# Optimization experiments

Measured on AMD Instinct MI355X. Metric: run time of the kernel, lower is better.

The kernel has to match this reference:

```python
import jax, jax.numpy as jnp
import numpy as np

# ---- static dims (from init_kwargs) ----
B, V, G, NH, C = 2, 3, 2, 8, 128
CPG, CH, HPG = C // G, C // NH, NH // G          # 64, 16, 4
Hq = Wq = 32
D = 4                                            # bev_depth_dim
Hk, Wk = Hq // 2, Wq * D                         # 16, 128 (per rearrange)
NS = Hk * Wk                                     # n_sample = 2048
Hi = Wi = 64
SCALE = CH ** -0.5
OFR = 5.0                                        # offset_range_factor
EPS = 1e-5


def grid_sample_bilinear(img, grid):
    """torch.F.grid_sample(mode='bilinear', align_corners=True, padding='zeros').
    img: (N, Cc, H, W); grid: (N, Hg, Wg, 2) with (x, y) in [-1, 1]."""
    N, Cc, H, W = img.shape
    x = (grid[..., 0] + 1.0) * 0.5 * (W - 1)
    y = (grid[..., 1] + 1.0) * 0.5 * (H - 1)
    x0 = jnp.floor(x); y0 = jnp.floor(y)
    wx1 = x - x0; wy1 = y - y0
    wx0 = 1.0 - wx1; wy0 = 1.0 - wy1

    def gather(ix, iy):
        valid = ((ix >= 0) & (ix <= W - 1) & (iy >= 0) & (iy <= H - 1)).astype(img.dtype)
        ixc = jnp.clip(ix, 0, W - 1).astype(jnp.int32)
        iyc = jnp.clip(iy, 0, H - 1).astype(jnp.int32)
        vals = jax.vmap(lambda im, yy, xx: im[:, yy, xx])(img, iyc, ixc)  # (N,Cc,Hg,Wg)
        return vals * valid[:, None]

    return (gather(x0, y0) * (wx0 * wy0)[:, None]
            + gather(x0 + 1.0, y0) * (wx1 * wy0)[:, None]
            + gather(x0, y0 + 1.0) * (wx0 * wy1)[:, None]
            + gather(x0 + 1.0, y0 + 1.0) * (wx1 * wy1)[:, None])


def offset_net(qg, w1, b1, gln, bln, w2):
    """Depthwise 1x1 conv (groups=CPG, fan-out D) -> channel LayerNorm -> GELU -> 1x1 conv.
    qg: (B*G, CPG, Hq, Wq) -> (B*G, D, Hq, Wq)."""
    h = qg[:, :, None] * w1.reshape(CPG, D)[None, :, :, None, None] \
        + b1.reshape(CPG, D)[None, :, :, None, None]
    h = h.reshape(B * G, CPG * D, Hq, Wq)
    mu = h.mean(axis=1, keepdims=True)
    var = h.var(axis=1, keepdims=True)           # biased, like torch LayerNorm
    h = (h - mu) * jax.lax.rsqrt(var + EPS) * gln[None, :, None, None] + bln[None, :, None, None]
    h = jax.nn.gelu(h, approximate=False)
    return jnp.einsum('oc,bchw->bohw', w2, h)


def _q_grid():
    gy, gx = jnp.meshgrid(jnp.linspace(-1.0, 1.0, Hq), jnp.linspace(-1.0, 1.0, Wq), indexing='ij')
    return jnp.stack([gy, gx], -1)               # (Hq, Wq, 2) in (y, x)


def setup_inputs() -> dict:
    key = jax.random.key(0)
    ks = jax.random.split(key, 15)
    s = 0.05
    return {
        'x': jax.random.normal(ks[0], (B, V, C, Hi, Wi), jnp.float32),
        'query': jax.random.normal(ks[1], (B, C, Hq, Wq), jnp.float32),
        'reference_points': jax.random.uniform(ks[2], (B, V, Hk, Wk, 2), jnp.float32) * 2.0 - 1.0,
        'off_w1': jax.random.normal(ks[3], (V, CPG * D), jnp.float32) * s,
        'off_b1': jax.random.normal(ks[4], (V, CPG * D), jnp.float32) * s,
        'off_ln_g': jnp.ones((V, CPG * D), jnp.float32),
        'off_ln_b': jnp.zeros((V, CPG * D), jnp.float32),
        'off_w2': jax.random.normal(ks[5], (V, D, CPG * D), jnp.float32) * s,
        'k_w': jax.random.normal(ks[6], (C, C), jnp.float32) * s,
        'k_b': jnp.zeros((C,), jnp.float32),
        'v_w': jax.random.normal(ks[7], (C, C), jnp.float32) * s,
        'v_b': jnp.zeros((C,), jnp.float32),
        'out_w': jax.random.normal(ks[8], (C, C * V), jnp.float32) * s,
        'out_b': jnp.zeros((C,), jnp.float32),
        'rpe_table': jax.random.normal(ks[9], (NH, Hq * 2 - 1, Wq * D * 2 - 1), jnp.float32) * 0.01,
    }


def reference(x, query, reference_points, off_w1, off_b1, off_ln_g, off_ln_b, off_w2,
              k_w, k_b, v_w, v_b, out_w, out_b, rpe_table):
    ref = reference_points[..., ::-1]                     # (x,y) -> (y,x)
    ref = jnp.repeat(ref, G, axis=0)                      # (B*G, V, Hk, Wk, 2)
    q_g = query.reshape(B, G, CPG, Hq, Wq).reshape(B * G, CPG, Hq, Wq)
    q = query.reshape(B * NH, CH, Hq * Wq)
    qg = _q_grid().reshape(1, Hq * Wq, 2)
    off_rng = jnp.array([1.0 / (Hk - 1.0), 1.0 / (Wk - 1.0)], jnp.float32).reshape(1, 2, 1, 1)
    rpe = jnp.broadcast_to(rpe_table[None], (B,) + rpe_table.shape)
    rpe = rpe.reshape(B * G, HPG, rpe_table.shape[1], rpe_table.shape[2])

    outs = []
    for vi in range(V):
        off = offset_net(q_g, off_w1[vi], off_b1[vi], off_ln_g[vi], off_ln_b[vi], off_w2[vi])
        # rearrange '(b g) d (h n) w -> (b g) n h (w d)'
        off = off.reshape(B * G, D, Hk, 2, Wq).transpose(0, 3, 2, 4, 1).reshape(B * G, 2, Hk, Wk)
        off = jnp.tanh(off) * off_rng * OFR
        off = off.transpose(0, 2, 3, 1)                   # (B*G, Hk, Wk, 2) in (y, x)
        rwo = off + ref[:, vi]                            # scale_offset_range=True -> no clamp
        xs = grid_sample_bilinear(x[:, vi].reshape(B * G, CPG, Hi, Wi), rwo[..., ::-1])
        xs = xs.reshape(B, C, NS)
        k = (jnp.einsum('oc,bcn->bon', k_w, xs) + k_b[None, :, None]).reshape(B * NH, CH, NS)
        vv = (jnp.einsum('oc,bcn->bon', v_w, xs) + v_b[None, :, None]).reshape(B * NH, CH, NS)
        attn = jnp.einsum('bcm,bcn->bmn', q, k) * SCALE   # (B*NH, m, NS)
        disp = (qg[:, :, None] - rwo.reshape(B * G, NS, 2)[:, None]) * 0.5  # (B*G, m, NS, 2)
        bias = grid_sample_bilinear(rpe, disp[..., ::-1]).reshape(B * NH, Hq * Wq, NS)
        attn = jax.nn.softmax(attn + bias, axis=-1)
        outs.append(jnp.einsum('bmn,bcn->bcm', attn, vv).reshape(B, C, Hq, Wq))

    out = jnp.concatenate(outs, axis=1)                   # (B, V*C, Hq, Wq)
    return jnp.einsum('oc,bchw->bohw', out_w, out) + out_b[None, :, None, None]
```

## Files before the change

kernel.cpp:

```cpp
#include <hip/hip_runtime.h>
#include <hip/hip_bf16.h>
#include <math.h>


typedef __attribute__((ext_vector_type(8))) short short8;
typedef __attribute__((ext_vector_type(4))) float f32x4;

__device__ __forceinline__ unsigned short f2b(float f){
  unsigned u = __float_as_uint(f);
  return (unsigned short)((u + 0x7FFFu + ((u>>16)&1u)) >> 16);
}
__device__ __forceinline__ unsigned pack2(float lo, float hi){
  return (unsigned)f2b(lo) | ((unsigned)f2b(hi) << 16);
}
__device__ __forceinline__ unsigned cvt_pk_bf16(float lo, float hi){
  unsigned r;
  asm("v_cvt_pk_bf16_f32 %0, %1, %2" : "=v"(r) : "v"(lo), "v"(hi));
  return r;
}

__global__ void k_probe(float* __restrict__ out, float code){
  if(blockIdx.x==0 && threadIdx.x==0) out[0] = code;
}

__global__ __launch_bounds__(256) void k_prep_off(
    const float* __restrict__ query, const float* __restrict__ refp,
    const float* __restrict__ w1, const float* __restrict__ b1,
    const float* __restrict__ lng, const float* __restrict__ lnb,
    const float* __restrict__ w2, float* __restrict__ rwo, float* __restrict__ rws,
    const float* __restrict__ x, float* __restrict__ xt,
    const float* __restrict__ k_w, const float* __restrict__ v_w, const float* __restrict__ out_w,
    unsigned short* __restrict__ kw16, unsigned short* __restrict__ vw16, float* __restrict__ ow_t){
  __shared__ float t[64][65];
  int bx = blockIdx.x;
  if(bx < 3072){
    int wid  = bx*4 + (threadIdx.x>>6);
    int lane = threadIdx.x & 63;
    int vi  = wid >> 12;
    int rem = wid & 4095;
    int bg  = rem >> 10;
    int pix = rem & 1023;
    int y = pix >> 5, xq = pix & 31;
    int b = bg >> 1, g = bg & 1;
    float qv = query[(size_t)(b*128 + g*64 + lane)*1024 + pix];
    float h[4]; float s1 = 0.f, s2 = 0.f;
    #pragma unroll
    for(int d=0; d<4; ++d){
      h[d] = qv*w1[vi*256 + lane*4 + d] + b1[vi*256 + lane*4 + d];
      s1 += h[d]; s2 += h[d]*h[d];
    }
    #pragma unroll
    for(int off=1; off<64; off<<=1){ s1 += __shfl_xor(s1, off); s2 += __shfl_xor(s2, off); }
    float mu   = s1 * (1.f/256.f);
    float var  = s2 * (1.f/256.f) - mu*mu;
    float rstd = rsqrtf(fmaxf(var, 0.f) + 1e-5f);
    float po[4] = {0.f,0.f,0.f,0.f};
    #pragma unroll
    for(int d=0; d<4; ++d){
      float hv = (h[d]-mu)*rstd*lng[vi*256+lane*4+d] + lnb[vi*256+lane*4+d];
      hv = 0.5f*hv*(1.f + erff(hv*0.70710678118654752f));
      #pragma unroll
      for(int o=0; o<4; ++o) po[o] += w2[(vi*4+o)*256 + lane*4 + d] * hv;
    }
    #pragma unroll
    for(int off=1; off<64; off<<=1){
      #pragma unroll
      for(int o=0; o<4; ++o) po[o] += __shfl_xor(po[o], off);
    }
    if(lane == 0){
      int tt = y & 1, hk = y >> 1;
      float rng = tt ? (5.f/127.f) : (5.f/15.f);
      float csc = tt ? 63.5f : 15.5f;
      #pragma unroll
      for(int d=0; d<4; ++d){
        int wk = xq*4 + d;
        float rv = refp[(size_t)(((b*3+vi)*16 + hk)*128 + wk)*2 + (1-tt)];
        float coord = tanhf(po[d])*rng + rv;
        size_t o2 = ((size_t)(vi*4+bg)*2048 + hk*128 + wk)*2 + tt;
        rwo[o2] = coord;
        rws[o2] = coord * csc;
      }
    }
  } else if(bx < 3840){
    int pb = bx - 3072;
    int iy = pb & 63;
    int o2 = pb >> 6;
    const float* src = x + ((size_t)o2*64)*4096 + (size_t)iy*64;
    int ix = threadIdx.x & 63, cq = threadIdx.x >> 6;
    #pragma unroll
    for(int c0 = 0; c0 < 64; c0 += 4)
      t[c0+cq][ix] = src[(size_t)(c0+cq)*4096 + ix];
    __syncthreads();
    float* dst = xt + (((size_t)o2*64 + iy)*64)*64;
    int c = threadIdx.x & 63, xq = threadIdx.x >> 6;
    #pragma unroll
    for(int x0 = 0; x0 < 64; x0 += 4)
      dst[(size_t)(x0+xq)*64 + c] = t[c][x0+xq];
  } else {
    int wb = bx - 3840;
    if(wb < 128){
      int i = (wb & 63)*256 + threadIdx.x;
      if(wb < 64) kw16[i] = f2b(k_w[i]);
      else        vw16[i] = f2b(v_w[i]);
    } else {
      int i = (wb-128)*256 + threadIdx.x;
      if(i < 49152){
        int r = i / 384, c = i - r*384;
        ow_t[c*128 + r] = out_w[i];
      }
    }
  }
}

__global__ __launch_bounds__(256) void k_sampro(
    const float* __restrict__ rwo, const float* __restrict__ xt,
    const unsigned short* __restrict__ kw16, const float* __restrict__ k_b,
    const unsigned short* __restrict__ vw16, const float* __restrict__ v_b,
    unsigned short* __restrict__ k_b16, unsigned short* __restrict__ v_t16){
  __shared__ alignas(16) unsigned short tile[16*136];
  int bx = blockIdx.x;
  int nt = bx & 127;
  int r2 = bx >> 7;
  int b = r2 & 1, vi = r2 >> 1;
  int n0 = nt*16;
  int tid = threadIdx.x, wid = tid>>6, lane = tid&63;
  #pragma unroll
  for(int s = 0; s < 8; ++s){
    int u = wid*8 + s;
    int nl = u >> 1, g = u & 1;
    int n = n0 + nl;
    float yn = rwo[((size_t)(vi*4 + b*2 + g)*2048 + n)*2 + 0];
    float xn = rwo[((size_t)(vi*4 + b*2 + g)*2048 + n)*2 + 1];
    float px = (xn + 1.f)*31.5f;
    float py = (yn + 1.f)*31.5f;
    float x0 = floorf(px), y0 = floorf(py);
    float fx = px - x0, fy = py - y0;
    int ix0 = (int)x0, iy0 = (int)y0;
    const float* base = xt + (size_t)((b*3+vi)*2+g)*4096*64;
    float wts[4] = {(1.f-fx)*(1.f-fy), fx*(1.f-fy), (1.f-fx)*fy, fx*fy};
    int ixs[4] = {ix0, ix0+1, ix0, ix0+1};
    int iys[4] = {iy0, iy0, iy0+1, iy0+1};
    float acc = 0.f;
    #pragma unroll
    for(int tp=0; tp<4; ++tp){
      int ix = ixs[tp], iy = iys[tp];
      if(ix>=0 && ix<64 && iy>=0 && iy<64)
        acc += wts[tp] * base[(size_t)((iy<<6)+ix)*64 + lane];
    }
    tile[nl*136 + g*64 + lane] = f2b(acc);
  }
  __syncthreads();
  int c = lane & 15, qd = lane >> 4;
  short8 af[4];
  #pragma unroll
  for(int kc=0; kc<4; ++kc)
    af[kc] = *(const short8*)(&tile[c*136 + kc*32 + qd*8]);
  size_t vbbase = (size_t)(vi*16 + b*8)*2048*16;
  const float SC2 = 0.36067376022224085f;
  int pbase = ((nt>>1)<<5) + (nt&1);
  #pragma unroll
  for(int half=0; half<2; ++half){
    int nh = wid*2 + half;
    size_t hbase = vbbase + (size_t)nh*2048*16;
    {
      f32x4 C = {0.f,0.f,0.f,0.f};
      #pragma unroll
      for(int kc=0; kc<4; ++kc){
        short8 bf = *(const short8*)(kw16 + (size_t)(nh*16 + c)*128 + kc*32 + qd*8);
        C = __builtin_amdgcn_mfma_f32_16x16x32_bf16(af[kc], bf, C, 0, 0, 0);
      }
      float bias = k_b[nh*16 + c];
      #pragma unroll
      for(int r=0; r<4; ++r)
        k_b16[hbase + (size_t)(n0 + qd*4 + r)*16 + c] = f2b((C[r] + bias)*SC2);
    }
    {
      f32x4 C = {0.f,0.f,0.f,0.f};
      #pragma unroll
      for(int kc=0; kc<4; ++kc){
        short8 bf = *(const short8*)(vw16 + (size_t)(nh*16 + c)*128 + kc*32 + qd*8);
        C = __builtin_amdgcn_mfma_f32_16x16x32_bf16(af[kc], bf, C, 0, 0, 0);
      }
      float bias = v_b[nh*16 + c];
      #pragma unroll
      for(int r=0; r<4; ++r)
        v_t16[hbase + (size_t)c*2048 + pbase + ((qd*4 + r)<<1)] = f2b(C[r] + bias);
    }
  }
}

__global__ __launch_bounds__(256,3) void k_attn(
    const float* __restrict__ rws, const unsigned short* __restrict__ k_b16,
    const unsigned short* __restrict__ v_t16, const float* __restrict__ query,
    const float* __restrict__ rpe, float* __restrict__ attn_pc){
  __shared__ unsigned P32[47*258];
  __shared__ alignas(16) short p_sm[4][16*40];
  int bx = blockIdx.x;
  int vi = bx >> 8;
  int bh = (bx >> 4) & 15;
  int mblk = bx & 15;
  int b = bh >> 3, nh = bh & 7, g = nh >> 2, bg = b*2 + g;
  int tid = threadIdx.x, wid = tid >> 6;
  int lane = tid & 63, c = lane & 15, qd = lane >> 4;
  int m0 = mblk*64 + wid*16;
  float gy0 = -1.f + (2.f/31.f)*(float)(mblk*2);
  float pyL = 15.5f*(gy0 - 4.f/3.f) + 31.f - 0.01f;
  float pyH = 15.5f*(gy0 + 2.f/31.f + 4.f/3.f) + 31.f + 0.01f;
  int a  = max(-1, (int)floorf(pyL));
  int bb = min(63, (int)floorf(pyH));
  int iy_lo = max(a - 1, bb - 46);
  {
    const float* rt = rpe + (size_t)nh*16065;
    for(int e = tid; e < 12126; e += 256){
      int rr = e / 258;
      int cc = e - rr*258;
      int iy = iy_lo + rr;
      int ix = cc - 1;
      bool xv = (ix >= 0) && (ix <= 254);
      float lo = (xv && iy   >= 0 && iy   <= 62) ? rt[iy*255 + ix]     : 0.f;
      float hi = (xv && iy+1 >= 0 && iy+1 <= 62) ? rt[(iy+1)*255 + ix] : 0.f;
      P32[e] = cvt_pk_bf16(lo*1.44269504f, hi*1.44269504f);
    }
  }
  short8 qa;
  #pragma unroll
  for(int j=0; j<8; ++j){
    int ch = qd*8 + j;
    qa[j] = (qd < 2) ? (short)f2b(query[(size_t)(b*128 + nh*16 + ch)*1024 + m0 + c]) : (short)0;
  }
  float Ax2[4];
  #pragma unroll
  for(int r=0; r<4; ++r){
    int mr = m0 + qd*4 + r;
    float gxr = -1.f + (2.f/31.f)*(mr & 31);
    Ax2[r] = 63.5f*gxr + 128.f;
  }
  float gyw = -1.f + (2.f/31.f)*(float)(m0 >> 5);
  float Ay  = 15.5f*gyw + 31.f - (float)iy_lo;
  float loC = -1.f - (float)iy_lo, hiC = 63.f - (float)iy_lo;
  float si[4] = {0.f, 0.f, 0.f, 0.f};
  f32x4 O = {0.f, 0.f, 0.f, 0.f};
  size_t kvb  = (size_t)(vi*16 + bh)*2048*16;
  size_t rwsb = (size_t)(vi*4 + bg)*2048;
  __syncthreads();
  for(int nc = 0; nc < 16; ++nc){
    int n0 = nc*128;
    f32x4 Sf[8];
    #pragma unroll
    for(int t=0; t<8; ++t){
      short8 bk = {0,0,0,0,0,0,0,0};
      if(qd < 2) bk = *(const short8*)(k_b16 + kvb + (size_t)(n0 + t*16 + c)*16 + qd*8);
      f32x4 z = {0.f,0.f,0.f,0.f};
      Sf[t] = __builtin_amdgcn_mfma_f32_16x16x32_bf16(qa, bk, z, 0, 0, 0);
    }
    float pf[8][4];
    #pragma unroll
    for(int t=0; t<8; ++t){
      float2 rs = *(const float2*)(rws + (rwsb + n0 + t*16 + c)*2);
      float py = Ay - rs.x;
      py = fminf(fmaxf(py, loC), hiC);
      float rf = floorf(py);
      float fy = py - rf;
      int rbase = (int)rf * 258;
      #pragma unroll
      for(int r=0; r<4; ++r){
        float px = Ax2[r] - rs.y;
        px = fminf(fmaxf(px, 0.f), 256.f);
        float cf = floorf(px);
        float fx = px - cf;
        int idx = rbase + (int)cf;
        unsigned w0 = P32[idx], w1 = P32[idx+1];
        float lo0 = __uint_as_float(w0 << 16), hi0 = __uint_as_float(w0 & 0xFFFF0000u);
        float lo1 = __uint_as_float(w1 << 16), hi1 = __uint_as_float(w1 & 0xFFFF0000u);
        float t0 = lo0 + fy*(hi0 - lo0);
        float t1 = lo1 + fy*(hi1 - lo1);
        float p = exp2f(Sf[t][r] + t0 + fx*(t1 - t0));
        si[r] += p;
        pf[t][r] = p;
      }
    }
    short* pw = &p_sm[wid][0];
    #pragma unroll
    for(int kc=0; kc<4; ++kc){
      #pragma unroll
      for(int r=0; r<4; ++r){
        unsigned pk = cvt_pk_bf16(pf[kc*2][r], pf[kc*2+1][r]);
        *(unsigned*)(&pw[(qd*4 + r)*40 + 2*c]) = pk;
      }
      short8 va = *(const short8*)(v_t16 + kvb + (size_t)c*2048 + n0 + kc*32 + qd*8);
      short8 pbf = *(const short8*)(&pw[c*40 + qd*8]);
      O = __builtin_amdgcn_mfma_f32_16x16x32_bf16(va, pbf, O, 0, 0, 0);
    }
  }
  #pragma unroll
  for(int r=0; r<4; ++r){
    float sv = si[r];
    sv += __shfl_xor(sv, 1); sv += __shfl_xor(sv, 2);
    sv += __shfl_xor(sv, 4); sv += __shfl_xor(sv, 8);
    si[r] = sv;
  }
  int msrc = (c >> 2)*16 + c;
  int rsel = c & 3;
  float s0 = __shfl(si[0], msrc), s1 = __shfl(si[1], msrc),
        s2 = __shfl(si[2], msrc), s3 = __shfl(si[3], msrc);
  float sv = (rsel==0) ? s0 : ((rsel==1) ? s1 : ((rsel==2) ? s2 : s3));
  float inv = 1.f/sv;
  float4 o4;
  o4.x = O[0]*inv; o4.y = O[1]*inv; o4.z = O[2]*inv; o4.w = O[3]*inv;
  *(float4*)(attn_pc + (size_t)(b*1024 + m0 + c)*384 + vi*128 + nh*16 + qd*4) = o4;
}

__global__ __launch_bounds__(256) void k_outproj(
    const float* __restrict__ attn_pc, const float* __restrict__ ow_t, const float* __restrict__ out_b,
    float* __restrict__ out){
  __shared__ float A[4*384];
  int bx = blockIdx.x;
  int b  = bx >> 8;
  int m0 = (bx & 255)*4;
  const float4* src = (const float4*)(attn_pc + ((size_t)b*1024 + m0)*384);
  float4* dst = (float4*)A;
  for(int i = threadIdx.x; i < 384; i += 256) dst[i] = src[i];
  __syncthreads();
  int oc = threadIdx.x & 127;
  int mh = threadIdx.x >> 7;
  float acc[2] = {0.f,0.f};
  #pragma unroll 4
  for(int vc = 0; vc < 384; ++vc){
    float wv = ow_t[vc*128 + oc];
    #pragma unroll
    for(int j=0; j<2; ++j) acc[j] += wv * A[(mh*2+j)*384 + vc];
  }
  float ob = out_b[oc];
  #pragma unroll
  for(int j=0; j<2; ++j)
    out[((size_t)b*128 + oc)*1024 + m0 + mh*2 + j] = acc[j] + ob;
}

extern "C" void kernel_launch(void* const* d_in, const int* in_sizes, int n_in,
                              void* d_out, int out_size, void* d_ws, size_t ws_size,
                              hipStream_t stream){
  const float* x     = (const float*)d_in[0];
  const float* query = (const float*)d_in[1];
  const float* refp  = (const float*)d_in[2];
  const float* w1    = (const float*)d_in[3];
  const float* b1    = (const float*)d_in[4];
  const float* lng   = (const float*)d_in[5];
  const float* lnb   = (const float*)d_in[6];
  const float* w2    = (const float*)d_in[7];
  const float* k_w   = (const float*)d_in[8];
  const float* k_b   = (const float*)d_in[9];
  const float* v_w   = (const float*)d_in[10];
  const float* v_b   = (const float*)d_in[11];
  const float* out_w = (const float*)d_in[12];
  const float* out_b = (const float*)d_in[13];
  const float* rpe   = (const float*)d_in[14];

  const size_t O_XT   = 0;
  const size_t O_RWO  = 12582912;
  const size_t O_RWS  = 12779520;
  const size_t O_KB16 = 12976128;
  const size_t O_VT16 = 16121856;
  const size_t O_APC  = 19267584;
  const size_t O_KW16 = 22413312;
  const size_t O_VW16 = 22446080;
  const size_t O_OWT  = 22478848;
  const size_t NEED   = 22675456;
  if(ws_size < NEED){
    k_probe<<<1, 64, 0, stream>>>((float*)d_out, 100.f + (float)(ws_size >> 20));
    return;
  }
  char* ws = (char*)d_ws;
  float* xt      = (float*)(ws + O_XT);
  float* rwo     = (float*)(ws + O_RWO);
  float* rws     = (float*)(ws + O_RWS);
  unsigned short* k_b16 = (unsigned short*)(ws + O_KB16);
  unsigned short* v_t16 = (unsigned short*)(ws + O_VT16);
  float* attn_pc = (float*)(ws + O_APC);
  unsigned short* kw16 = (unsigned short*)(ws + O_KW16);
  unsigned short* vw16 = (unsigned short*)(ws + O_VW16);
  float* ow_t    = (float*)(ws + O_OWT);

  k_prep_off<<<4160, 256, 0, stream>>>(query, refp, w1, b1, lng, lnb, w2, rwo, rws,
                                       x, xt, k_w, v_w, out_w, kw16, vw16, ow_t);
  k_sampro  <<<768,  256, 0, stream>>>(rwo, xt, kw16, k_b, vw16, v_b, k_b16, v_t16);
  k_attn    <<<768,  256, 0, stream>>>(rws, k_b16, v_t16, query, rpe, attn_pc);
  k_outproj <<<512,  256, 0, stream>>>(attn_pc, ow_t, out_b, (float*)d_out);
}
```

Baseline: 273.8 us.

## Split attention key range across two wave groups and reduce partial sums in LDS

k_attn now runs 512 threads per block: eight waves, where two groups each cover half of the 2048 samples for the same query rows. The partial output and softmax sums are combined through LDS at the end. This amortises the per-block RPE table staging over more waves and adds parallelism, at the cost of an extra reduction and higher register and LDS pressure. The RPE table is also padded to 263 columns to reduce bank conflicts and stores the row difference to save a subtraction. The V projection store in k_sampro changes to a packed, contiguous layout, and the P tile writes are adjusted to match.

```diff
diff --git a/kernel.cpp b/kernel.cpp
--- a/kernel.cpp
+++ b/kernel.cpp
@@ -9,9 +9,6 @@
 __device__ __forceinline__ unsigned short f2b(float f){
   unsigned u = __float_as_uint(f);
   return (unsigned short)((u + 0x7FFFu + ((u>>16)&1u)) >> 16);
-}
-__device__ __forceinline__ unsigned pack2(float lo, float hi){
-  return (unsigned)f2b(lo) | ((unsigned)f2b(hi) << 16);
 }
 __device__ __forceinline__ unsigned cvt_pk_bf16(float lo, float hi){
   unsigned r;
@@ -157,7 +154,6 @@
     af[kc] = *(const short8*)(&tile[c*136 + kc*32 + qd*8]);
   size_t vbbase = (size_t)(vi*16 + b*8)*2048*16;
   const float SC2 = 0.36067376022224085f;
-  int pbase = ((nt>>1)<<5) + (nt&1);
   #pragma unroll
   for(int half=0; half<2; ++half){
     int nh = wid*2 + half;
@@ -182,27 +178,30 @@
         C = __builtin_amdgcn_mfma_f32_16x16x32_bf16(af[kc], bf, C, 0, 0, 0);
       }
       float bias = v_b[nh*16 + c];
-      #pragma unroll
-      for(int r=0; r<4; ++r)
-        v_t16[hbase + (size_t)c*2048 + pbase + ((qd*4 + r)<<1)] = f2b(C[r] + bias);
-    }
-  }
-}
-
-__global__ __launch_bounds__(256,3) void k_attn(
+      uint2 pk;
+      pk.x = cvt_pk_bf16(C[0]+bias, C[1]+bias);
+      pk.y = cvt_pk_bf16(C[2]+bias, C[3]+bias);
+      *(uint2*)(v_t16 + hbase + (size_t)c*2048 + n0 + qd*4) = pk;
+    }
+  }
+}
+
+__global__ __launch_bounds__(512,4) void k_attn(
     const float* __restrict__ rws, const unsigned short* __restrict__ k_b16,
     const unsigned short* __restrict__ v_t16, const float* __restrict__ query,
     const float* __restrict__ rpe, float* __restrict__ attn_pc){
-  __shared__ unsigned P32[47*258];
-  __shared__ alignas(16) short p_sm[4][16*40];
+  __shared__ unsigned P32[47*263];
+  __shared__ alignas(16) short p_sm[8][16*40];
   int bx = blockIdx.x;
   int vi = bx >> 8;
   int bh = (bx >> 4) & 15;
   int mblk = bx & 15;
   int b = bh >> 3, nh = bh & 7, g = nh >> 2, bg = b*2 + g;
   int tid = threadIdx.x, wid = tid >> 6;
+  int w4 = wid & 3;
+  int nhf = wid >> 2;
   int lane = tid & 63, c = lane & 15, qd = lane >> 4;
-  int m0 = mblk*64 + wid*16;
+  int m0 = mblk*64 + w4*16;
   float gy0 = -1.f + (2.f/31.f)*(float)(mblk*2);
   float pyL = 15.5f*(gy0 - 4.f/3.f) + 31.f - 0.01f;
   float pyH = 15.5f*(gy0 + 2.f/31.f + 4.f/3.f) + 31.f + 0.01f;
@@ -211,15 +210,17 @@
   int iy_lo = max(a - 1, bb - 46);
   {
     const float* rt = rpe + (size_t)nh*16065;
-    for(int e = tid; e < 12126; e += 256){
-      int rr = e / 258;
-      int cc = e - rr*258;
-      int iy = iy_lo + rr;
-      int ix = cc - 1;
-      bool xv = (ix >= 0) && (ix <= 254);
-      float lo = (xv && iy   >= 0 && iy   <= 62) ? rt[iy*255 + ix]     : 0.f;
-      float hi = (xv && iy+1 >= 0 && iy+1 <= 62) ? rt[(iy+1)*255 + ix] : 0.f;
-      P32[e] = cvt_pk_bf16(lo*1.44269504f, hi*1.44269504f);
+    for(int e = tid; e < 47*263; e += 512){
+      int rr = e / 263;
+      int cc = e - rr*263;
+      if(cc < 258){
+        int iy = iy_lo + rr;
+        int ix = cc - 1;
+        bool xv = (ix >= 0) && (ix <= 254);
+        float lo = (xv && iy   >= 0 && iy   <= 62) ? rt[iy*255 + ix]     : 0.f;
+        float hi = (xv && iy+1 >= 0 && iy+1 <= 62) ? rt[(iy+1)*255 + ix] : 0.f;
+        P32[e] = cvt_pk_bf16(lo*1.44269504f, (hi - lo)*1.44269504f);
+      }
     }
   }
   short8 qa;
@@ -237,13 +238,14 @@
   }
   float gyw = -1.f + (2.f/31.f)*(float)(m0 >> 5);
   float Ay  = 15.5f*gyw + 31.f - (float)iy_lo;
-  float loC = -1.f - (float)iy_lo, hiC = 63.f - (float)iy_lo;
+  float loC = fmaxf(-1.f - (float)iy_lo, 0.f);
+  float hiC = fminf(63.f - (float)iy_lo, 45.f);
   float si[4] = {0.f, 0.f, 0.f, 0.f};
   f32x4 O = {0.f, 0.f, 0.f, 0.f};
   size_t kvb  = (size_t)(vi*16 + bh)*2048*16;
   size_t rwsb = (size_t)(vi*4 + bg)*2048;
   __syncthreads();
-  for(int nc = 0; nc < 16; ++nc){
+  for(int nc = nhf*8, ncE = nhf*8 + 8; nc < ncE; ++nc){
     int n0 = nc*128;
     f32x4 Sf[8];
     #pragma unroll
@@ -261,7 +263,7 @@
       py = fminf(fmaxf(py, loC), hiC);
       float rf = floorf(py);
       float fy = py - rf;
-      int rbase = (int)rf * 258;
+      int rbase = (int)rf * 263;
       #pragma unroll
       for(int r=0; r<4; ++r){
         float px = Ax2[r] - rs.y;
@@ -270,10 +272,10 @@
         float fx = px - cf;
         int idx = rbase + (int)cf;
         unsigned w0 = P32[idx], w1 = P32[idx+1];
-        float lo0 = __uint_as_float(w0 << 16), hi0 = __uint_as_float(w0 & 0xFFFF0000u);
-        float lo1 = __uint_as_float(w1 << 16), hi1 = __uint_as_float(w1 & 0xFFFF0000u);
-        float t0 = lo0 + fy*(hi0 - lo0);
-        float t1 = lo1 + fy*(hi1 - lo1);
+        float lo0 = __uint_as_float(w0 << 16), d0 = __uint_as_float(w0 & 0xFFFF0000u);
+        float lo1 = __uint_as_float(w1 << 16), d1 = __uint_as_float(w1 & 0xFFFF0000u);
+        float t0 = lo0 + fy*d0;
+        float t1 = lo1 + fy*d1;
         float p = exp2f(Sf[t][r] + t0 + fx*(t1 - t0));
         si[r] += p;
         pf[t][r] = p;
@@ -285,29 +287,46 @@
       #pragma unroll
       for(int r=0; r<4; ++r){
         unsigned pk = cvt_pk_bf16(pf[kc*2][r], pf[kc*2+1][r]);
-        *(unsigned*)(&pw[(qd*4 + r)*40 + 2*c]) = pk;
+        pw[(qd*4 + r)*40 + c]      = (short)pk;
+        pw[(qd*4 + r)*40 + 16 + c] = (short)(pk >> 16);
       }
       short8 va = *(const short8*)(v_t16 + kvb + (size_t)c*2048 + n0 + kc*32 + qd*8);
       short8 pbf = *(const short8*)(&pw[c*40 + qd*8]);
       O = __builtin_amdgcn_mfma_f32_16x16x32_bf16(va, pbf, O, 0, 0, 0);
     }
   }
-  #pragma unroll
-  for(int r=0; r<4; ++r){
-    float sv = si[r];
-    sv += __shfl_xor(sv, 1); sv += __shfl_xor(sv, 2);
-    sv += __shfl_xor(sv, 4); sv += __shfl_xor(sv, 8);
-    si[r] = sv;
-  }
-  int msrc = (c >> 2)*16 + c;
-  int rsel = c & 3;
-  float s0 = __shfl(si[0], msrc), s1 = __shfl(si[1], msrc),
-        s2 = __shfl(si[2], msrc), s3 = __shfl(si[3], msrc);
-  float sv = (rsel==0) ? s0 : ((rsel==1) ? s1 : ((rsel==2) ? s2 : s3));
-  float inv = 1.f/sv;
-  float4 o4;
-  o4.x = O[0]*inv; o4.y = O[1]*inv; o4.z = O[2]*inv; o4.w = O[3]*inv;
-  *(float4*)(attn_pc + (size_t)(b*1024 + m0 + c)*384 + vi*128 + nh*16 + qd*4) = o4;
+  __syncthreads();
+  float* red = (float*)&p_sm[0][0];
+  int basei = (w4*64 + lane)*8;
+  if(nhf){
+    red[basei+0] = O[0];  red[basei+1] = O[1];
+    red[basei+2] = O[2];  red[basei+3] = O[3];
+    red[basei+4] = si[0]; red[basei+5] = si[1];
+    red[basei+6] = si[2]; red[basei+7] = si[3];
+  }
+  __syncthreads();
+  if(!nhf){
+    O[0] += red[basei+0]; O[1] += red[basei+1];
+    O[2] += red[basei+2]; O[3] += red[basei+3];
+    si[0] += red[basei+4]; si[1] += red[basei+5];
+    si[2] += red[basei+6]; si[3] += red[basei+7];
+    #pragma unroll
+    for(int r=0; r<4; ++r){
+      float sv = si[r];
+      sv += __shfl_xor(sv, 1); sv += __shfl_xor(sv, 2);
+      sv += __shfl_xor(sv, 4); sv += __shfl_xor(sv, 8);
+      si[r] = sv;
+    }
+    int msrc = (c >> 2)*16 + c;
+    int rsel = c & 3;
+    float s0 = __shfl(si[0], msrc), s1 = __shfl(si[1], msrc),
+          s2 = __shfl(si[2], msrc), s3 = __shfl(si[3], msrc);
+    float sv = (rsel==0) ? s0 : ((rsel==1) ? s1 : ((rsel==2) ? s2 : s3));
+    float inv = 1.f/sv;
+    float4 o4;
+    o4.x = O[0]*inv; o4.y = O[1]*inv; o4.z = O[2]*inv; o4.w = O[3]*inv;
+    *(float4*)(attn_pc + (size_t)(b*1024 + m0 + c)*384 + vi*128 + nh*16 + qd*4) = o4;
+  }
 }
 
 __global__ __launch_bounds__(256) void k_outproj(
@@ -383,6 +402,6 @@
   k_prep_off<<<4160, 256, 0, stream>>>(query, refp, w1, b1, lng, lnb, w2, rwo, rws,
                                        x, xt, k_w, v_w, out_w, kw16, vw16, ow_t);
   k_sampro  <<<768,  256, 0, stream>>>(rwo, xt, kw16, k_b, vw16, v_b, k_b16, v_t16);
-  k_attn    <<<768,  256, 0, stream>>>(rws, k_b16, v_t16, query, rpe, attn_pc);
+  k_attn    <<<768,  512, 0, stream>>>(rws, k_b16, v_t16, query, rpe, attn_pc);
   k_outproj <<<512,  256, 0, stream>>>(attn_pc, ow_t, out_b, (float*)d_out);
 }
```

Result: faster. 257.5 us (-6.0%).
